# Performance work log

Hardware: AMD Instinct MI355X
Metric: run time of the kernel (lower is better)

Reference implementation:

```python
import jax, jax.numpy as jnp
import numpy as np

N_NODES = 50000
N_EDGES = 1600000
IN_FEATURES = 128
D_ATT = 64
N_HEADS = 8
D_HEAD = D_ATT // N_HEADS
EPS = 1e-16  # torch_geometric softmax eps


def setup_inputs() -> dict:
    key = jax.random.key(0)
    ks = jax.random.split(key, 9)
    return {
        "x": jax.random.normal(ks[0], (N_NODES, IN_FEATURES), dtype=jnp.float32),
        "Wq": jax.random.normal(ks[1], (D_ATT, IN_FEATURES), dtype=jnp.float32) * 0.02,
        "bq": jax.random.normal(ks[2], (D_ATT,), dtype=jnp.float32) * 0.02,
        "Wk": jax.random.normal(ks[3], (D_ATT, IN_FEATURES), dtype=jnp.float32) * 0.02,
        "bk": jax.random.normal(ks[4], (D_ATT,), dtype=jnp.float32) * 0.02,
        "Wv": jax.random.normal(ks[5], (D_ATT, IN_FEATURES), dtype=jnp.float32) * 0.02,
        "bv": jax.random.normal(ks[6], (D_ATT,), dtype=jnp.float32) * 0.02,
        "edge_attr": jax.random.uniform(ks[7], (N_EDGES,), dtype=jnp.float32),
        "edge": jax.random.randint(ks[8], (2, N_EDGES), 0, N_NODES, dtype=jnp.int64),
    }


def segment_softmax(logits, seg, num_segments):
    # logits: (E, H), seg: (E,) destination-node ids
    m = jax.ops.segment_max(logits, seg, num_segments=num_segments)  # (N, H)
    ex = jnp.exp(logits - m[seg])
    s = jax.ops.segment_sum(ex, seg, num_segments=num_segments)      # (N, H)
    return ex / (s[seg] + EPS)


def reference(x, Wq, bq, Wk, bk, Wv, bv, edge_attr, edge):
    n = x.shape[0]
    # Linear projections, reshape to (N, n_heads, d_head) then transpose(1,2) -> (N, d_head, n_heads)
    q = (x @ Wq.T + bq).reshape(n, N_HEADS, D_HEAD).transpose(0, 2, 1)
    k = (x @ Wk.T + bk).reshape(n, N_HEADS, D_HEAD).transpose(0, 2, 1)
    v = (x @ Wv.T + bv).reshape(n, N_HEADS, D_HEAD).transpose(0, 2, 1)
    src = q[edge[0]]     # (E, d_head, n_heads)
    dst_k = k[edge[1]]   # (E, d_head, n_heads)
    prods = jnp.sum(src * dst_k, axis=1) / np.sqrt(D_HEAD).astype(np.float32)  # (E, n_heads)
    # reweight_attention=True with per-edge scalar edge_attr
    prods = prods * edge_attr[:, None]
    # square_plus=False -> segment softmax grouped by edge[attention_norm_idx=1]
    attention = segment_softmax(prods, edge[1], N_NODES)
    return attention, v, prods
```

## Files before the change

kernel.cpp:

```cpp
#include <hip/hip_runtime.h>
#include <hip/hip_bf16.h>
#include <math.h>

#define N_NODES   50000
#define N_EDGES   1600000
#define IN_F      128
#define D_ATT     64
#define N_HEADS   8
#define D_HEAD    8
#define RSQRT8    0.35355339059327373f
#define EPS_SM    1e-16f
#define NEH       (N_EDGES * N_HEADS)

__device__ inline unsigned short f2bf(float v) {
    __hip_bfloat16 b = __float2bfloat16(v);
    return *(unsigned short*)&b;
}
__device__ inline float bflo(unsigned u) { return __uint_as_float(u << 16); }
__device__ inline float bfhi(unsigned u) { return __uint_as_float(u & 0xffff0000u); }

__global__ __launch_bounds__(256) void k_proj(
        const float* __restrict__ x,
        const float* __restrict__ Wq, const float* __restrict__ bq,
        const float* __restrict__ Wk, const float* __restrict__ bk,
        const float* __restrict__ Wv, const float* __restrict__ bv,
        unsigned short* __restrict__ qp, unsigned short* __restrict__ kp,
        float* __restrict__ vout, float* __restrict__ s) {
    __shared__ float Xs[128][64];
    __shared__ float Ws[128][64];
    const int tid = threadIdx.x;
    const int n0  = blockIdx.x * 64;
    const int ln  = tid & 63;
    const int kb  = tid >> 6;

    {
        int nthr = gridDim.x * 256;
        for (int i = blockIdx.x * 256 + tid; i < N_NODES * N_HEADS; i += nthr)
            s[i] = 0.0f;
    }

    {
        int n = n0 + ln;
        if (n < N_NODES) {
            const float4* xr = (const float4*)(x + (size_t)n * IN_F + kb * 32);
#pragma unroll
            for (int i = 0; i < 8; ++i) {
                float4 v = xr[i];
                int k = kb * 32 + i * 4;
                Xs[k + 0][ln] = v.x; Xs[k + 1][ln] = v.y;
                Xs[k + 2][ln] = v.z; Xs[k + 3][ln] = v.w;
            }
        } else {
#pragma unroll
            for (int i = 0; i < 8; ++i) {
                int k = kb * 32 + i * 4;
                Xs[k + 0][ln] = 0.f; Xs[k + 1][ln] = 0.f;
                Xs[k + 2][ln] = 0.f; Xs[k + 3][ln] = 0.f;
            }
        }
    }

    const int tx = tid & 15;
    const int ty = tid >> 4;

    const float* Wlist[3] = {Wq, Wk, Wv};
    const float* blist[3] = {bq, bk, bv};

    for (int mm = 0; mm < 3; ++mm) {
        __syncthreads();
        {
            const float4* wr = (const float4*)(Wlist[mm] + (size_t)ln * IN_F + kb * 32);
#pragma unroll
            for (int i = 0; i < 8; ++i) {
                float4 v = wr[i];
                int k = kb * 32 + i * 4;
                Ws[k + 0][ln] = v.x; Ws[k + 1][ln] = v.y;
                Ws[k + 2][ln] = v.z; Ws[k + 3][ln] = v.w;
            }
        }
        __syncthreads();

        float acc[4][4] = {};
#pragma unroll 4
        for (int kk = 0; kk < 128; ++kk) {
            float4 a = *(const float4*)&Xs[kk][tx * 4];
            float4 b = *(const float4*)&Ws[kk][ty * 4];
            float xr[4] = {a.x, a.y, a.z, a.w};
            float wr[4] = {b.x, b.y, b.z, b.w};
#pragma unroll
            for (int i = 0; i < 4; ++i)
#pragma unroll
                for (int j = 0; j < 4; ++j)
                    acc[i][j] += xr[i] * wr[j];
        }

        float bj[4];
#pragma unroll
        for (int j = 0; j < 4; ++j) bj[j] = blist[mm][ty * 4 + j];

#pragma unroll
        for (int i = 0; i < 4; ++i) {
            int nn = n0 + tx * 4 + i;
            if (nn >= N_NODES) continue;
            if (mm < 2) {
                unsigned short* dstp = (mm == 0 ? qp : kp) + (size_t)nn * 64 + ty * 4;
                ushort4 o;
                o.x = f2bf(acc[i][0] + bj[0]);
                o.y = f2bf(acc[i][1] + bj[1]);
                o.z = f2bf(acc[i][2] + bj[2]);
                o.w = f2bf(acc[i][3] + bj[3]);
                *(ushort4*)dstp = o;
            } else {
#pragma unroll
                for (int j = 0; j < 4; ++j) {
                    int jj = ty * 4 + j;
                    vout[(size_t)nn * 64 + (jj & 7) * 8 + (jj >> 3)] =
                        acc[i][j] + bj[j];
                }
            }
        }
    }
}

__global__ void k_prods_exp(const int* __restrict__ e0, const int* __restrict__ e1,
                            const float* __restrict__ ea,
                            const unsigned short* __restrict__ qp,
                            const unsigned short* __restrict__ kp,
                            float* __restrict__ prods_out,
                            float* __restrict__ s) {
    int t = blockIdx.x * blockDim.x + threadIdx.x;
    if (t >= NEH) return;
    int e = t >> 3, h = t & 7;
    int src = e0[e];
    int dst = e1[e];
    float w = ea[e] * RSQRT8;
    uint4 qv = *(const uint4*)(qp + (size_t)src * 64 + h * 8);
    uint4 kv = *(const uint4*)(kp + (size_t)dst * 64 + h * 8);
    float dot = bflo(qv.x) * bflo(kv.x) + bfhi(qv.x) * bfhi(kv.x)
              + bflo(qv.y) * bflo(kv.y) + bfhi(qv.y) * bfhi(kv.y)
              + bflo(qv.z) * bflo(kv.z) + bfhi(qv.z) * bfhi(kv.z)
              + bflo(qv.w) * bflo(kv.w) + bfhi(qv.w) * bfhi(kv.w);
    float p = dot * w;
    prods_out[t] = p;
    atomicAdd(&s[(size_t)dst * 8 + h], __expf(p));
}

__global__ void k_norm(const int* __restrict__ e1,
                       const float* __restrict__ prods,
                       float* __restrict__ att,
                       const float* __restrict__ s) {
    int t = blockIdx.x * blockDim.x + threadIdx.x;
    if (t >= NEH) return;
    int e = t >> 3, h = t & 7;
    int dst = e1[e];
    att[t] = __expf(prods[t]) / (s[(size_t)dst * 8 + h] + EPS_SM);
}

extern "C" void kernel_launch(void* const* d_in, const int* in_sizes, int n_in,
                              void* d_out, int out_size, void* d_ws, size_t ws_size,
                              hipStream_t stream) {
    const float* x  = (const float*)d_in[0];
    const float* Wq = (const float*)d_in[1];
    const float* bq = (const float*)d_in[2];
    const float* Wk = (const float*)d_in[3];
    const float* bk = (const float*)d_in[4];
    const float* Wv = (const float*)d_in[5];
    const float* bv = (const float*)d_in[6];
    const float* ea = (const float*)d_in[7];
    const int*   edge = (const int*)d_in[8];
    const int* e0 = edge;
    const int* e1 = edge + N_EDGES;

    float* out   = (float*)d_out;
    float* att   = out;
    float* vout  = att + (size_t)NEH;
    float* prods = vout + (size_t)N_NODES * D_ATT;

    unsigned short* qp = (unsigned short*)d_ws;
    unsigned short* kp = qp + (size_t)N_NODES * D_ATT;
    float* ssum = (float*)(kp + (size_t)N_NODES * D_ATT);

    const int B = 256;
    int nTiles = (N_NODES + 63) / 64;
    k_proj<<<nTiles, 256, 0, stream>>>(x, Wq, bq, Wk, bk, Wv, bv,
                                       qp, kp, vout, ssum);

    int nEH = NEH;
    k_prods_exp<<<(nEH + B - 1) / B, B, 0, stream>>>(e0, e1, ea, qp, kp,
                                                     prods, ssum);

    k_norm<<<(nEH + B - 1) / B, B, 0, stream>>>(e1, prods, att, ssum);
}
```

Measured before the change: 301.2 us.

## Fuse edge logits and normalization into one cooperative kernel with grid sync

Replaces the two edge kernels with a single persistent cooperative kernel. Each thread keeps its 49 exp values in registers across a grid-wide barrier, so the second pass no longer re-reads prods from memory or recomputes exp. Outputs are written with nontemporal stores. The cost is a grid sync and heavy register use from 49 live values with an occupancy requirement of 4 blocks per CU; the old two-kernel path is kept as a fallback.

```diff
diff --git a/kernel.cpp b/kernel.cpp
--- a/kernel.cpp
+++ b/kernel.cpp
@@ -1,4 +1,5 @@
 #include <hip/hip_runtime.h>
+#include <hip/hip_cooperative_groups.h>
 #include <hip/hip_bf16.h>
 #include <math.h>
 
@@ -11,6 +12,11 @@
 #define RSQRT8    0.35355339059327373f
 #define EPS_SM    1e-16f
 #define NEH       (N_EDGES * N_HEADS)
+
+#define GRID_F    1024
+#define THR_F     256
+#define STRIDE_F  (GRID_F * THR_F)
+#define ITEMS     49
 
 __device__ inline unsigned short f2bf(float v) {
     __hip_bfloat16 b = __float2bfloat16(v);
@@ -118,6 +124,55 @@
                         acc[i][j] + bj[j];
                 }
             }
+        }
+    }
+}
+
+__global__ __launch_bounds__(THR_F, 4) void k_fused(
+        const int* __restrict__ e0, const int* __restrict__ e1,
+        const float* __restrict__ ea,
+        const unsigned short* __restrict__ qp,
+        const unsigned short* __restrict__ kp,
+        float* __restrict__ prods_out,
+        float* __restrict__ s,
+        float* __restrict__ att) {
+    const int base = blockIdx.x * THR_F + threadIdx.x;
+    float ep[ITEMS];
+
+#pragma unroll
+    for (int i = 0; i < ITEMS; ++i) {
+        int t = base + i * STRIDE_F;
+        if (t < NEH) {
+            int e = t >> 3, h = t & 7;
+            int src = e0[e];
+            int dst = e1[e];
+            float w = ea[e] * RSQRT8;
+            uint4 qv = *(const uint4*)(qp + (size_t)src * 64 + h * 8);
+            uint4 kv = *(const uint4*)(kp + (size_t)dst * 64 + h * 8);
+            float dot = bflo(qv.x) * bflo(kv.x) + bfhi(qv.x) * bfhi(kv.x)
+                      + bflo(qv.y) * bflo(kv.y) + bfhi(qv.y) * bfhi(kv.y)
+                      + bflo(qv.z) * bflo(kv.z) + bfhi(qv.z) * bfhi(kv.z)
+                      + bflo(qv.w) * bflo(kv.w) + bfhi(qv.w) * bfhi(kv.w);
+            float p = dot * w;
+            __builtin_nontemporal_store(p, &prods_out[t]);
+            float ev = __expf(p);
+            ep[i] = ev;
+            atomicAdd(&s[(size_t)dst * 8 + h], ev);
+        } else {
+            ep[i] = 0.0f;
+        }
+    }
+
+    cooperative_groups::this_grid().sync();
+
+#pragma unroll
+    for (int i = 0; i < ITEMS; ++i) {
+        int t = base + i * STRIDE_F;
+        if (t < NEH) {
+            int e = t >> 3, h = t & 7;
+            int dst = e1[e];
+            float a = ep[i] / (s[(size_t)dst * 8 + h] + EPS_SM);
+            __builtin_nontemporal_store(a, &att[t]);
         }
     }
 }
@@ -185,9 +240,28 @@
     k_proj<<<nTiles, 256, 0, stream>>>(x, Wq, bq, Wk, bk, Wv, bv,
                                        qp, kp, vout, ssum);
 
-    int nEH = NEH;
-    k_prods_exp<<<(nEH + B - 1) / B, B, 0, stream>>>(e0, e1, ea, qp, kp,
-                                                     prods, ssum);
-
-    k_norm<<<(nEH + B - 1) / B, B, 0, stream>>>(e1, prods, att, ssum);
-}
+    static int use_coop = -1;
+    if (use_coop < 0) {
+        int nb = 0;
+        hipError_t err = hipOccupancyMaxActiveBlocksPerMultiprocessor(
+                &nb, k_fused, THR_F, 0);
+        use_coop = (err == hipSuccess && nb >= 4) ? 1 : 0;
+    }
+
+    bool launched = false;
+    if (use_coop) {
+        void* args[] = {(void*)&e0, (void*)&e1, (void*)&ea, (void*)&qp,
+                        (void*)&kp, (void*)&prods, (void*)&ssum, (void*)&att};
+        hipError_t err = hipLaunchCooperativeKernel(
+                k_fused, dim3(GRID_F), dim3(THR_F), args, 0, stream);
+        if (err == hipSuccess) launched = true;
+        else use_coop = 0;
+    }
+
+    if (!launched) {
+        int nEH = NEH;
+        k_prods_exp<<<(nEH + B - 1) / B, B, 0, stream>>>(e0, e1, ea, qp, kp,
+                                                         prods, ssum);
+        k_norm<<<(nEH + B - 1) / B, B, 0, stream>>>(e1, prods, att, ssum);
+    }
+}
```

New measurement: 304.0 us. Within noise of the previous version (+0.9%).
